# Performance work log

Hardware: AMD Instinct MI355X
Metric: run time of the kernel (lower is better)

The kernel has to match this reference:

```python
import jax, jax.numpy as jnp
import numpy as np

B, T, V, F = 64, 2, 512, 512  # V == F required by the original loop indexing

def setup_inputs() -> dict:
    key = jax.random.key(0)
    x = jax.random.normal(key, (B, T, V, F), dtype=jnp.float32)
    return {"x": x}

def reference(x):
    # split along time axis into two halves; only the first slice of the first half is used
    xh, _ = jnp.split(x, 2, axis=1)
    x0 = xh[:, 0]  # (B, V, F)
    # Faithful to tf.norm(x[:, 0, i, :], ord=2) with NO axis: Frobenius norm over
    # the whole (batch, feature) slice -> one scalar per vertex.
    n = jnp.sqrt(jnp.sum(x0 * x0, axis=(0, 2)))  # (V,)
    # S[b,i,j] = sum_f x0[b,i,f] * x0[b,j,f]  (inner loop over j covers all V since V==F)
    gram = jnp.einsum('bif,bjf->bij', x0, x0)  # (B, V, V)
    return gram / (n[:, None] * n[None, :])
```

## Files before the change

kernel.cpp:

```cpp
#include <hip/hip_runtime.h>
#include <hip/hip_bf16.h>
#include <math.h>


#define BATCH 64
#define VDIM 512
#define FDIM 512
#define XBS (2 * VDIM * FDIM)
#define OBS (VDIM * VDIM)

typedef __bf16 bf16x8 __attribute__((ext_vector_type(8)));
typedef __bf16 bf16x4 __attribute__((ext_vector_type(4)));
typedef float f32x4 __attribute__((ext_vector_type(4)));

#define BM 128
#define BK 64

#define NSQ_OFF 33554432

#define GLL16(g, l)                                                          \
    __builtin_amdgcn_global_load_lds(                                        \
        (const __attribute__((address_space(1))) void*)(g),                  \
        (__attribute__((address_space(3))) void*)(l), 16, 0, 0)

__global__ __launch_bounds__(256) void cvt_norm_kernel(const float* __restrict__ x,
                                                       __bf16* __restrict__ xb,
                                                       float* __restrict__ nsq) {
    const int bid = blockIdx.x;
    const int L = (bid & 7) * 128 + (bid >> 3);
    const int b = L >> 4;
    const int g = L & 15;
    const int tid = threadIdx.x;
    const int r = tid >> 3;
    const int seg = tid & 7;

    const f32x4* src = (const f32x4*)(x + (size_t)b * XBS + (size_t)(g * 32) * FDIM);
    bf16x4* dst = (bf16x4*)(xb + (size_t)b * (VDIM * FDIM) + (size_t)(g * 32) * FDIM);

    float s = 0.f;
    #pragma unroll
    for (int k = 0; k < 16; ++k) {
        int c = r * 128 + seg + k * 8;
        f32x4 d = src[c];
        s += d[0] * d[0] + d[1] * d[1] + d[2] * d[2] + d[3] * d[3];
        bf16x4 p;
        p[0] = (__bf16)d[0]; p[1] = (__bf16)d[1]; p[2] = (__bf16)d[2]; p[3] = (__bf16)d[3];
        dst[c] = p;
    }
    s += __shfl_xor(s, 1, 64);
    s += __shfl_xor(s, 2, 64);
    s += __shfl_xor(s, 4, 64);
    __shared__ float nl[32];
    if (seg == 0) nl[r] = s;
    __syncthreads();
    if (tid < 32) atomicAdd(&nsq[g * 32 + tid], nl[tid]);
}

__global__ __launch_bounds__(256) void gram_kernel(const __bf16* __restrict__ xb,
                                                   const float* __restrict__ nsq,
                                                   float* __restrict__ out) {
    __shared__ __bf16 As[BM * BK];
    __shared__ __bf16 Bs[BM * BK];

    const int bid = blockIdx.x;
    const int wg = (bid & 7) * 128 + (bid >> 3);
    const int batch = wg >> 4;
    const int tile = wg & 15;
    const int ti = tile >> 2;
    const int tj = tile & 3;

    const __bf16* xbb = xb + (size_t)batch * (VDIM * FDIM);
    const int tid = threadIdx.x;
    const int lane = tid & 63;
    const int wave = tid >> 6;
    const int wr = wave >> 1;
    const int wc = wave & 1;

    const __bf16* gA[4];
    const __bf16* gB[4];
    __bf16* la[4];
    __bf16* lb[4];
    #pragma unroll
    for (int it = 0; it < 4; ++it) {
        int c = it * 256 + tid;
        int row = c >> 3;
        int cs = (c & 7) ^ (row & 7);
        gA[it] = xbb + (size_t)(ti * BM + row) * FDIM + cs * 8;
        gB[it] = xbb + (size_t)(tj * BM + row) * FDIM + cs * 8;
        la[it] = &As[c * 8];
        lb[it] = &Bs[c * 8];
    }

    int offA[2][4], offB[2][4];
    #pragma unroll
    for (int ks = 0; ks < 2; ++ks) {
        #pragma unroll
        for (int m = 0; m < 4; ++m) {
            int rA = wr * 64 + m * 16 + (lane & 15);
            int rB = wc * 64 + m * 16 + (lane & 15);
            int gch = ks * 4 + (lane >> 4);
            offA[ks][m] = rA * (BK * 2) + ((gch ^ (rA & 7)) * 16);
            offB[ks][m] = rB * (BK * 2) + ((gch ^ (rB & 7)) * 16);
        }
    }

    f32x4 acc[4][4];
    #pragma unroll
    for (int m = 0; m < 4; ++m)
        #pragma unroll
        for (int n = 0; n < 4; ++n)
            acc[m][n] = (f32x4){0.f, 0.f, 0.f, 0.f};

    for (int kk = 0; kk < FDIM; kk += BK) {
        #pragma unroll
        for (int it = 0; it < 4; ++it) {
            GLL16(gA[it] + kk, la[it]);
            GLL16(gB[it] + kk, lb[it]);
        }
        __syncthreads();

        #pragma unroll
        for (int ks = 0; ks < 2; ++ks) {
            bf16x8 af[4], bfr[4];
            #pragma unroll
            for (int m = 0; m < 4; ++m) {
                af[m]  = *(const bf16x8*)((const char*)As + offA[ks][m]);
                bfr[m] = *(const bf16x8*)((const char*)Bs + offB[ks][m]);
            }
            #pragma unroll
            for (int m = 0; m < 4; ++m)
                #pragma unroll
                for (int n = 0; n < 4; ++n)
                    acc[m][n] = __builtin_amdgcn_mfma_f32_16x16x32_bf16(af[m], bfr[n], acc[m][n], 0, 0, 0);
        }
        __syncthreads();
    }

    const int rowbase = ti * BM + wr * 64;
    const int colbase = tj * BM + wc * 64;
    float* ob = out + (size_t)batch * OBS;

    float si[16];
    #pragma unroll
    for (int m = 0; m < 4; ++m)
        #pragma unroll
        for (int q = 0; q < 4; ++q)
            si[m * 4 + q] = rsqrtf(nsq[rowbase + m * 16 + (lane >> 4) * 4 + q]);

    #pragma unroll
    for (int n = 0; n < 4; ++n) {
        int j = colbase + n * 16 + (lane & 15);
        float sj = rsqrtf(nsq[j]);
        #pragma unroll
        for (int m = 0; m < 4; ++m) {
            #pragma unroll
            for (int q = 0; q < 4; ++q) {
                int i = rowbase + m * 16 + (lane >> 4) * 4 + q;
                ob[(size_t)i * VDIM + j] = acc[m][n][q] * si[m * 4 + q] * sj;
            }
        }
    }
}

extern "C" void kernel_launch(void* const* d_in, const int* in_sizes, int n_in,
                              void* d_out, int out_size, void* d_ws, size_t ws_size,
                              hipStream_t stream) {
    const float* x = (const float*)d_in[0];
    float* out = (float*)d_out;
    __bf16* xbf = (__bf16*)d_ws;
    float* nsq = (float*)((char*)d_ws + NSQ_OFF);

    hipMemsetAsync(nsq, 0, VDIM * sizeof(float), stream);
    cvt_norm_kernel<<<BATCH * 16, 256, 0, stream>>>(x, xbf, nsq);
    gram_kernel<<<BATCH * 16, 256, 0, stream>>>(xbf, nsq, out);
}
```

Baseline: 51.23 us.

## Fuse convert-norm and gram kernels with per-batch flag synchronization

Merges the bf16 conversion/norm kernel and the gram GEMM kernel into one launch. The first 256 blocks act as producers, converting slabs and raising per-batch flags. The remaining blocks spin on their batch flag before the GEMM, then wait for a global counter before applying the norm scaling. This removes one launch boundary and lets GEMM work overlap with conversion. It relies on producer blocks being scheduled ahead of consumers, and uses a bounded spin to avoid hanging.

```diff
diff --git a/kernel.cpp b/kernel.cpp
--- a/kernel.cpp
+++ b/kernel.cpp
@@ -8,6 +8,7 @@
 #define FDIM 512
 #define XBS (2 * VDIM * FDIM)
 #define OBS (VDIM * VDIM)
+#define VF (VDIM * FDIM)
 
 typedef __bf16 bf16x8 __attribute__((ext_vector_type(8)));
 typedef __bf16 bf16x4 __attribute__((ext_vector_type(4)));
@@ -17,60 +18,77 @@
 #define BK 64
 
 #define NSQ_OFF 33554432
+#define FLAG_OFF (NSQ_OFF + 2048)
+#define NCNT_OFF (FLAG_OFF + 256)
 
 #define GLL16(g, l)                                                          \
     __builtin_amdgcn_global_load_lds(                                        \
         (const __attribute__((address_space(1))) void*)(g),                  \
         (__attribute__((address_space(3))) void*)(l), 16, 0, 0)
 
-__global__ __launch_bounds__(256) void cvt_norm_kernel(const float* __restrict__ x,
-                                                       __bf16* __restrict__ xb,
-                                                       float* __restrict__ nsq) {
-    const int bid = blockIdx.x;
-    const int L = (bid & 7) * 128 + (bid >> 3);
-    const int b = L >> 4;
-    const int g = L & 15;
-    const int tid = threadIdx.x;
-    const int r = tid >> 3;
-    const int seg = tid & 7;
-
-    const f32x4* src = (const f32x4*)(x + (size_t)b * XBS + (size_t)(g * 32) * FDIM);
-    bf16x4* dst = (bf16x4*)(xb + (size_t)b * (VDIM * FDIM) + (size_t)(g * 32) * FDIM);
-
-    float s = 0.f;
-    #pragma unroll
-    for (int k = 0; k < 16; ++k) {
-        int c = r * 128 + seg + k * 8;
-        f32x4 d = src[c];
-        s += d[0] * d[0] + d[1] * d[1] + d[2] * d[2] + d[3] * d[3];
-        bf16x4 p;
-        p[0] = (__bf16)d[0]; p[1] = (__bf16)d[1]; p[2] = (__bf16)d[2]; p[3] = (__bf16)d[3];
-        dst[c] = p;
-    }
-    s += __shfl_xor(s, 1, 64);
-    s += __shfl_xor(s, 2, 64);
-    s += __shfl_xor(s, 4, 64);
-    __shared__ float nl[32];
-    if (seg == 0) nl[r] = s;
-    __syncthreads();
-    if (tid < 32) atomicAdd(&nsq[g * 32 + tid], nl[tid]);
-}
-
-__global__ __launch_bounds__(256) void gram_kernel(const __bf16* __restrict__ xb,
-                                                   const float* __restrict__ nsq,
-                                                   float* __restrict__ out) {
+__global__ __launch_bounds__(256) void fused_kernel(const float* __restrict__ x,
+                                                    __bf16* __restrict__ ws,
+                                                    float* __restrict__ nsq,
+                                                    unsigned* __restrict__ slabflag,
+                                                    unsigned* __restrict__ ncnt,
+                                                    float* __restrict__ out) {
     __shared__ __bf16 As[BM * BK];
     __shared__ __bf16 Bs[BM * BK];
 
     const int bid = blockIdx.x;
-    const int wg = (bid & 7) * 128 + (bid >> 3);
-    const int batch = wg >> 4;
-    const int tile = wg & 15;
+    const int tid = threadIdx.x;
+
+    if (bid < 256) {
+        const int r = tid >> 3;
+        const int seg = tid & 7;
+        #pragma unroll
+        for (int t = 0; t < 4; ++t) {
+            const int slab = t * 256 + bid;
+            const int b = slab >> 4;
+            const int g = slab & 15;
+            const f32x4* src = (const f32x4*)(x + (size_t)b * XBS + (size_t)(g * 32) * FDIM);
+            bf16x4* dst = (bf16x4*)(ws + (size_t)b * VF + (size_t)(g * 32) * FDIM);
+            float s = 0.f;
+            #pragma unroll
+            for (int k = 0; k < 16; ++k) {
+                int c = r * 128 + seg + k * 8;
+                f32x4 d = src[c];
+                s += d[0] * d[0] + d[1] * d[1] + d[2] * d[2] + d[3] * d[3];
+                bf16x4 p;
+                p[0] = (__bf16)d[0]; p[1] = (__bf16)d[1];
+                p[2] = (__bf16)d[2]; p[3] = (__bf16)d[3];
+                dst[c] = p;
+            }
+            s += __shfl_xor(s, 1, 64);
+            s += __shfl_xor(s, 2, 64);
+            s += __shfl_xor(s, 4, 64);
+            if (seg == 0) atomicAdd(&nsq[g * 32 + r], s);
+            __syncthreads();
+            if (tid == 0)
+                __hip_atomic_fetch_add(&slabflag[b], 1u, __ATOMIC_RELEASE,
+                                       __HIP_MEMORY_SCOPE_AGENT);
+        }
+        if (tid == 0)
+            __hip_atomic_fetch_add(ncnt, 1u, __ATOMIC_RELEASE,
+                                   __HIP_MEMORY_SCOPE_AGENT);
+        return;
+    }
+
+    const int c = bid - 256;
+    const int batch = c >> 4;
+    const int tile = c & 15;
     const int ti = tile >> 2;
     const int tj = tile & 3;
 
-    const __bf16* xbb = xb + (size_t)batch * (VDIM * FDIM);
-    const int tid = threadIdx.x;
+    if (tid == 0) {
+        int fuse = 1 << 24;
+        while (__hip_atomic_load(&slabflag[batch], __ATOMIC_ACQUIRE,
+                                 __HIP_MEMORY_SCOPE_AGENT) < 16u && --fuse)
+            __builtin_amdgcn_s_sleep(8);
+    }
+    __syncthreads();
+
+    const __bf16* xbb = ws + (size_t)batch * VF;
     const int lane = tid & 63;
     const int wave = tid >> 6;
     const int wr = wave >> 1;
@@ -82,13 +100,13 @@
     __bf16* lb[4];
     #pragma unroll
     for (int it = 0; it < 4; ++it) {
-        int c = it * 256 + tid;
-        int row = c >> 3;
-        int cs = (c & 7) ^ (row & 7);
+        int c2 = it * 256 + tid;
+        int row = c2 >> 3;
+        int cs = (c2 & 7) ^ (row & 7);
         gA[it] = xbb + (size_t)(ti * BM + row) * FDIM + cs * 8;
         gB[it] = xbb + (size_t)(tj * BM + row) * FDIM + cs * 8;
-        la[it] = &As[c * 8];
-        lb[it] = &Bs[c * 8];
+        la[it] = &As[c2 * 8];
+        lb[it] = &Bs[c2 * 8];
     }
 
     int offA[2][4], offB[2][4];
@@ -136,6 +154,14 @@
         __syncthreads();
     }
 
+    if (tid == 0) {
+        int fuse = 1 << 24;
+        while (__hip_atomic_load(ncnt, __ATOMIC_ACQUIRE,
+                                 __HIP_MEMORY_SCOPE_AGENT) < 256u && --fuse)
+            __builtin_amdgcn_s_sleep(8);
+    }
+    __syncthreads();
+
     const int rowbase = ti * BM + wr * 64;
     const int colbase = tj * BM + wc * 64;
     float* ob = out + (size_t)batch * OBS;
@@ -167,10 +193,11 @@
                               hipStream_t stream) {
     const float* x = (const float*)d_in[0];
     float* out = (float*)d_out;
-    __bf16* xbf = (__bf16*)d_ws;
+    __bf16* ws = (__bf16*)d_ws;
     float* nsq = (float*)((char*)d_ws + NSQ_OFF);
-
-    hipMemsetAsync(nsq, 0, VDIM * sizeof(float), stream);
-    cvt_norm_kernel<<<BATCH * 16, 256, 0, stream>>>(x, xbf, nsq);
-    gram_kernel<<<BATCH * 16, 256, 0, stream>>>(xbf, nsq, out);
+    unsigned* slabflag = (unsigned*)((char*)d_ws + FLAG_OFF);
+    unsigned* ncnt = (unsigned*)((char*)d_ws + NCNT_OFF);
+
+    hipMemsetAsync(nsq, 0, 2560, stream);
+    fused_kernel<<<1280, 256, 0, stream>>>(x, ws, nsq, slabflag, ncnt, out);
 }
```

New measurement: 117.9 us. +130.1%, slower.
